# Kernel tuning notes

Measured on AMD Instinct MI355X. Metric: run time of the kernel, lower is better.

## Reference

```python
import jax, jax.numpy as jnp
import numpy as np

TEMPERATURE = 0.5
EPS = 1e-8  # torch.nn.CosineSimilarity default eps


def setup_inputs() -> dict:
    key = jax.random.key(0)
    k1, k2 = jax.random.split(key)
    B, D = 4096, 256
    z1 = jax.random.normal(k1, (B, D), dtype=jnp.float32)
    # z2 = perturbed view of z1 so positive cosine sims are positive
    # (original torch code takes log of the RAW cosine sim, which is NaN
    #  for negative positives; realistic SimCLR positives are correlated views)
    z2 = z1 + 0.1 * jax.random.normal(k2, (B, D), dtype=jnp.float32)
    return {"z1": z1, "z2": z2}


def reference(z1, z2):
    B = z1.shape[0]
    z = jnp.concatenate([z1, z2], axis=0)                      # [2B, D]
    norm = jnp.maximum(jnp.linalg.norm(z, axis=-1, keepdims=True), EPS)
    zn = z / norm
    sim = zn @ zn.T                                            # [2B, 2B] cosine sims
    # positives: sim[i, i+B] and sim[i+B, i] (RAW cosine, per original code)
    pos = jnp.concatenate([jnp.diagonal(sim, offset=B),
                           jnp.diagonal(sim, offset=-B)])      # [2B]
    # mask self-similarity diagonal to -inf before exp-sum
    diag = jnp.eye(2 * B, dtype=bool)
    sim_masked = jnp.where(diag, -jnp.inf, sim)
    denom = jnp.sum(jnp.exp(sim_masked / TEMPERATURE), axis=-1)  # [2B]
    loss = -jnp.mean(jnp.log(pos / denom))
    return loss
```

## Files before the change

kernel.cpp:

```cpp
#include <hip/hip_runtime.h>
#include <hip/hip_bf16.h>


#define NROWS 8192
#define BHALF 4096
#define DDIM  256

typedef __attribute__((ext_vector_type(4))) int   i32x4;
typedef __attribute__((ext_vector_type(8))) int   i32x8;
typedef __attribute__((ext_vector_type(4))) float f32x4;

#define SCALE1 0x7F7F7F7F
#define TWO_LOG2E 2.8853900817779268f

__device__ __forceinline__ void load_lds16(const unsigned char* g, unsigned char* l) {
    __builtin_amdgcn_global_load_lds(
        (const __attribute__((address_space(1))) void*)g,
        (__attribute__((address_space(3))) void*)l, 16, 0, 0);
}

__global__ __launch_bounds__(256) void prep_kernel(const float* __restrict__ z1,
                                                   const float* __restrict__ z2,
                                                   unsigned char* __restrict__ zn8,
                                                   float* __restrict__ posPart,
                                                   float* __restrict__ denom) {
    __shared__ float sp[4];
    int wave = threadIdx.x >> 6;
    int lane = threadIdx.x & 63;
    int i    = blockIdx.x * 4 + wave;
    float4 a = reinterpret_cast<const float4*>(z1 + (size_t)i * DDIM)[lane];
    float4 b = reinterpret_cast<const float4*>(z2 + (size_t)i * DDIM)[lane];
    float ss1 = a.x * a.x + a.y * a.y + a.z * a.z + a.w * a.w;
    float ss2 = b.x * b.x + b.y * b.y + b.z * b.z + b.w * b.w;
    float dd  = a.x * b.x + a.y * b.y + a.z * b.z + a.w * b.w;
    #pragma unroll
    for (int off = 32; off; off >>= 1) {
        ss1 += __shfl_xor(ss1, off);
        ss2 += __shfl_xor(ss2, off);
        dd  += __shfl_xor(dd, off);
    }
    float n1 = fmaxf(sqrtf(ss1), 1e-8f);
    float n2 = fmaxf(sqrtf(ss2), 1e-8f);
    float i1 = 1.0f / n1, i2 = 1.0f / n2;
    int pa = __builtin_amdgcn_cvt_pk_fp8_f32(a.x * i1, a.y * i1, 0, 0);
    pa     = __builtin_amdgcn_cvt_pk_fp8_f32(a.z * i1, a.w * i1, pa, 1);
    int pb = __builtin_amdgcn_cvt_pk_fp8_f32(b.x * i2, b.y * i2, 0, 0);
    pb     = __builtin_amdgcn_cvt_pk_fp8_f32(b.z * i2, b.w * i2, pb, 1);
    reinterpret_cast<int*>(zn8 + (size_t)i * DDIM)[lane] = pa;
    reinterpret_cast<int*>(zn8 + (size_t)(i + BHALF) * DDIM)[lane] = pb;
    if (lane == 0) sp[wave] = __logf(dd * i1 * i2);
    if (threadIdx.x < 8) denom[blockIdx.x * 8 + threadIdx.x] = 0.0f;
    __syncthreads();
    if (threadIdx.x == 0)
        posPart[blockIdx.x] = sp[0] + sp[1] + sp[2] + sp[3];
}

__global__ __launch_bounds__(256, 2) void denom_kernel(const unsigned char* __restrict__ zn8,
                                                       float* __restrict__ denom) {
    __shared__ __align__(16) unsigned char sA[128 * DDIM];
    __shared__ __align__(16) unsigned char sB[128 * DDIM];

    int t    = threadIdx.x;
    int lane = t & 63;
    int wave = t >> 6;
    int col  = lane & 15;
    int quad = lane >> 4;
    int wm = wave >> 1, wn = wave & 1;
    int iBase = blockIdx.y * 128;
    int jBase = blockIdx.x * 128;

    int rowL  = t >> 4;
    int chunk = (t & 15) ^ rowL;
    const unsigned char* gA = zn8 + (size_t)(iBase + rowL) * DDIM + chunk * 16;
    const unsigned char* gB = zn8 + (size_t)(jBase + rowL) * DDIM + chunk * 16;
    unsigned char* lA = sA + t * 16;
    unsigned char* lB = sB + t * 16;
    #pragma unroll
    for (int s = 0; s < 8; s++) {
        load_lds16(gA + s * 4096, lA + s * 4096);
        load_lds16(gB + s * 4096, lB + s * 4096);
    }
    __syncthreads();

    i32x8 bfr[4][2];
    {
        const unsigned char* bRow = sB + (size_t)(wn * 64 + col) * DDIM;
        #pragma unroll
        for (int nt = 0; nt < 4; nt++) {
            #pragma unroll
            for (int ks = 0; ks < 2; ks++) {
                int g0 = ks * 8 + quad * 2;
                i32x4 lo = *(const i32x4*)(bRow + nt * 16 * DDIM + ((g0    ) ^ col) * 16);
                i32x4 hi = *(const i32x4*)(bRow + nt * 16 * DDIM + ((g0 + 1) ^ col) * 16);
                bfr[nt][ks] = __builtin_shufflevector(lo, hi, 0, 1, 2, 3, 4, 5, 6, 7);
            }
        }
    }

    float rs[4][4];
    #pragma unroll
    for (int mt = 0; mt < 4; mt++)
        #pragma unroll
        for (int r = 0; r < 4; r++) rs[mt][r] = 0.f;

    const unsigned char* aRow = sA + (size_t)(wm * 64 + col) * DDIM;
    #pragma unroll
    for (int mt = 0; mt < 4; mt++) {
        i32x8 af[2];
        #pragma unroll
        for (int ks = 0; ks < 2; ks++) {
            int g0 = ks * 8 + quad * 2;
            i32x4 lo = *(const i32x4*)(aRow + mt * 16 * DDIM + ((g0    ) ^ col) * 16);
            i32x4 hi = *(const i32x4*)(aRow + mt * 16 * DDIM + ((g0 + 1) ^ col) * 16);
            af[ks] = __builtin_shufflevector(lo, hi, 0, 1, 2, 3, 4, 5, 6, 7);
        }
        int gi = iBase + wm * 64 + mt * 16;
        #pragma unroll
        for (int nt = 0; nt < 4; nt++) {
            f32x4 acc = {0.f, 0.f, 0.f, 0.f};
            acc = __builtin_amdgcn_mfma_scale_f32_16x16x128_f8f6f4(
                      af[0], bfr[nt][0], acc, 0, 0, 0, SCALE1, 0, SCALE1);
            acc = __builtin_amdgcn_mfma_scale_f32_16x16x128_f8f6f4(
                      af[1], bfr[nt][1], acc, 0, 0, 0, SCALE1, 0, SCALE1);
            bool dtile = (gi == jBase + wn * 64 + nt * 16);
            #pragma unroll
            for (int r = 0; r < 4; r++) {
                float e = exp2f(acc[r] * TWO_LOG2E);
                if (dtile && (quad * 4 + r) == col) e = 0.f;
                rs[mt][r] += e;
            }
        }
    }

    #pragma unroll
    for (int mt = 0; mt < 4; mt++)
        #pragma unroll
        for (int r = 0; r < 4; r++) {
            float x = rs[mt][r];
            x += __shfl_xor(x, 1);
            x += __shfl_xor(x, 2);
            x += __shfl_xor(x, 4);
            x += __shfl_xor(x, 8);
            rs[mt][r] = x;
        }
    __syncthreads();
    float* red = (float*)sA;
    if (col == 0) {
        #pragma unroll
        for (int mt = 0; mt < 4; mt++)
            #pragma unroll
            for (int r = 0; r < 4; r++)
                red[wn * 128 + wm * 64 + mt * 16 + quad * 4 + r] = rs[mt][r];
    }
    __syncthreads();
    if (t < 128)
        atomicAdd(&denom[iBase + t], red[t] + red[128 + t]);
}

__global__ __launch_bounds__(256) void loss_kernel(const float* __restrict__ posPart,
                                                   const float* __restrict__ denom,
                                                   float* __restrict__ out) {
    __shared__ float sdata[4];
    int t = threadIdx.x;
    float s = __logf(denom[blockIdx.x * 256 + t]);
    if (t < 32) s -= 2.0f * posPart[blockIdx.x * 32 + t];
    #pragma unroll
    for (int off = 32; off; off >>= 1) s += __shfl_xor(s, off);
    if ((t & 63) == 0) sdata[t >> 6] = s;
    __syncthreads();
    if (t == 0)
        atomicAdd(out, (sdata[0] + sdata[1] + sdata[2] + sdata[3]) * (1.0f / NROWS));
}

extern "C" void kernel_launch(void* const* d_in, const int* in_sizes, int n_in,
                              void* d_out, int out_size, void* d_ws, size_t ws_size,
                              hipStream_t stream) {
    const float* z1 = (const float*)d_in[0];
    const float* z2 = (const float*)d_in[1];

    unsigned char* zn8 = (unsigned char*)d_ws;
    float* denom   = (float*)((char*)d_ws + (size_t)NROWS * DDIM);
    float* posPart = denom + NROWS;

    hipMemsetAsync(d_out, 0, sizeof(float), stream);
    prep_kernel<<<BHALF / 4, 256, 0, stream>>>(z1, z2, zn8, posPart, denom);
    denom_kernel<<<dim3(NROWS / 128, NROWS / 128), 256, 0, stream>>>(zn8, denom);
    loss_kernel<<<NROWS / 256, 256, 0, stream>>>(posPart, denom, (float*)d_out);
}
```

Baseline: 106.4 us.

## Exploit symmetry of similarity matrix to compute only upper-triangular tiles

The similarity matrix is symmetric, so the denominator kernel now launches only the upper-triangular block pairs (65x32 grid mapped to i<=j tiles). Each off-diagonal tile adds its row sums to the i rows and its column sums to the j rows, which roughly halves the MFMA and exp work. The output zeroing moves into the prep kernel, removing a separate memset launch. In exchange it adds column-sum shuffles and more atomics per tile.

```diff
diff --git a/kernel.cpp b/kernel.cpp
--- a/kernel.cpp
+++ b/kernel.cpp
@@ -23,7 +23,8 @@
                                                    const float* __restrict__ z2,
                                                    unsigned char* __restrict__ zn8,
                                                    float* __restrict__ posPart,
-                                                   float* __restrict__ denom) {
+                                                   float* __restrict__ denom,
+                                                   float* __restrict__ out) {
     __shared__ float sp[4];
     int wave = threadIdx.x >> 6;
     int lane = threadIdx.x & 63;
@@ -50,6 +51,7 @@
     reinterpret_cast<int*>(zn8 + (size_t)(i + BHALF) * DDIM)[lane] = pb;
     if (lane == 0) sp[wave] = __logf(dd * i1 * i2);
     if (threadIdx.x < 8) denom[blockIdx.x * 8 + threadIdx.x] = 0.0f;
+    if (blockIdx.x == 0 && threadIdx.x == 64) out[0] = 0.0f;
     __syncthreads();
     if (threadIdx.x == 0)
         posPart[blockIdx.x] = sp[0] + sp[1] + sp[2] + sp[3];
@@ -59,6 +61,14 @@
                                                        float* __restrict__ denom) {
     __shared__ __align__(16) unsigned char sA[128 * DDIM];
     __shared__ __align__(16) unsigned char sB[128 * DDIM];
+
+    int x = blockIdx.x, y = blockIdx.y;
+    int bi, bj;
+    if (x > y) { bi = y;      bj = x - 1;  }
+    else       { bi = 63 - y; bj = 63 - x; }
+    int iBase = bi * 128;
+    int jBase = bj * 128;
+    bool isDiag = (bi == bj);
 
     int t    = threadIdx.x;
     int lane = t & 63;
@@ -66,8 +76,6 @@
     int col  = lane & 15;
     int quad = lane >> 4;
     int wm = wave >> 1, wn = wave & 1;
-    int iBase = blockIdx.y * 128;
-    int jBase = blockIdx.x * 128;
 
     int rowL  = t >> 4;
     int chunk = (t & 15) ^ rowL;
@@ -98,6 +106,7 @@
     }
 
     float rs[4][4];
+    float cs[4] = {0.f, 0.f, 0.f, 0.f};
     #pragma unroll
     for (int mt = 0; mt < 4; mt++)
         #pragma unroll
@@ -123,12 +132,26 @@
             acc = __builtin_amdgcn_mfma_scale_f32_16x16x128_f8f6f4(
                       af[1], bfr[nt][1], acc, 0, 0, 0, SCALE1, 0, SCALE1);
             bool dtile = (gi == jBase + wn * 64 + nt * 16);
+            float csl = 0.f;
             #pragma unroll
             for (int r = 0; r < 4; r++) {
                 float e = exp2f(acc[r] * TWO_LOG2E);
                 if (dtile && (quad * 4 + r) == col) e = 0.f;
                 rs[mt][r] += e;
+                csl += e;
             }
+            cs[nt] += csl;
+        }
+    }
+
+    if (!isDiag) {
+        #pragma unroll
+        for (int nt = 0; nt < 4; nt++) {
+            float v = cs[nt];
+            v += __shfl_xor(v, 16);
+            v += __shfl_xor(v, 32);
+            if (quad == 0)
+                atomicAdd(&denom[jBase + wn * 64 + nt * 16 + col], v);
         }
     }
 
@@ -136,12 +159,12 @@
     for (int mt = 0; mt < 4; mt++)
         #pragma unroll
         for (int r = 0; r < 4; r++) {
-            float x = rs[mt][r];
-            x += __shfl_xor(x, 1);
-            x += __shfl_xor(x, 2);
-            x += __shfl_xor(x, 4);
-            x += __shfl_xor(x, 8);
-            rs[mt][r] = x;
+            float v = rs[mt][r];
+            v += __shfl_xor(v, 1);
+            v += __shfl_xor(v, 2);
+            v += __shfl_xor(v, 4);
+            v += __shfl_xor(v, 8);
+            rs[mt][r] = v;
         }
     __syncthreads();
     float* red = (float*)sA;
@@ -182,8 +205,7 @@
     float* denom   = (float*)((char*)d_ws + (size_t)NROWS * DDIM);
     float* posPart = denom + NROWS;
 
-    hipMemsetAsync(d_out, 0, sizeof(float), stream);
-    prep_kernel<<<BHALF / 4, 256, 0, stream>>>(z1, z2, zn8, posPart, denom);
-    denom_kernel<<<dim3(NROWS / 128, NROWS / 128), 256, 0, stream>>>(zn8, denom);
+    prep_kernel<<<BHALF / 4, 256, 0, stream>>>(z1, z2, zn8, posPart, denom, (float*)d_out);
+    denom_kernel<<<dim3(65, 32), 256, 0, stream>>>(zn8, denom);
     loss_kernel<<<NROWS / 256, 256, 0, stream>>>(posPart, denom, (float*)d_out);
 }
```

After: 89.27 us. 1.19x faster.
